# Kernel tuning notes

Measured on AMD Instinct MI355X. Metric: run time of the kernel, lower is better.

Reference implementation:

```python
import jax, jax.numpy as jnp
import numpy as np

TEMPERATURE = 0.5
EPS = 1e-8  # torch CosineSimilarity eps


def setup_inputs() -> dict:
    key = jax.random.key(0)
    k1, k2 = jax.random.split(key)
    N, D = 4096, 256
    z1 = jax.random.normal(k1, (N, D), dtype=jnp.float32)
    z2 = jax.random.normal(k2, (N, D), dtype=jnp.float32)
    return {"z1": z1, "z2": z2}


def reference(z1, z2):
    N = z1.shape[0]
    z = jnp.concatenate([z1, z2], axis=0)  # [2N, D]
    # cosine similarity = normalized dot products (GEMM instead of O(N^2 D) broadcast)
    norm = jnp.linalg.norm(z, axis=-1, keepdims=True)
    zn = z / jnp.maximum(norm, EPS)
    sim = (zn @ zn.T) / TEMPERATURE  # [2N, 2N]
    # mask self-similarity on the diagonal
    idx = jnp.arange(2 * N)
    sim = jnp.where(idx[:, None] == idx[None, :], -jnp.inf, sim)
    # target[i] = (i - N) mod 2N  (arange(2N).roll(N))
    target = jnp.roll(idx, N)
    logp = jax.nn.log_softmax(sim, axis=-1)
    loss = -jnp.mean(logp[idx, target])
    return loss
```

## Files before the change

### kernel.cpp

```cpp
#include <hip/hip_runtime.h>

typedef __bf16 bf16x8 __attribute__((ext_vector_type(8)));
typedef float f32x4 __attribute__((ext_vector_type(4)));

#define TWO_LOG2E 2.88539008177792681f

#define GLOADLDS16(g, l) __builtin_amdgcn_global_load_lds(                     \
    (const __attribute__((address_space(1))) void*)(g),                        \
    (__attribute__((address_space(3))) void*)(l), 16, 0, 0)

__device__ __forceinline__ unsigned f2bf(float f) {
    unsigned u = __float_as_uint(f);
    return (u + 0x7FFFu + ((u >> 16) & 1u)) >> 16;
}

__global__ void __launch_bounds__(256) normalize_kernel(
    const float* __restrict__ z1, const float* __restrict__ z2,
    unsigned short* __restrict__ zn, float* __restrict__ S, float* __restrict__ out)
{
    if (blockIdx.x < 32) S[(blockIdx.x << 8) + threadIdx.x] = 0.f;
    if (blockIdx.x == 32 && threadIdx.x == 0) out[0] = 0.f;

    const int wave = threadIdx.x >> 6, lane = threadIdx.x & 63;
    const int row = (blockIdx.x << 2) + wave;
    const float* src = (row < 4096) ? (z1 + row * 256) : (z2 + (row - 4096) * 256);
    float4 v = ((const float4*)src)[lane];
    float ss = v.x * v.x + v.y * v.y + v.z * v.z + v.w * v.w;
#pragma unroll
    for (int m = 32; m > 0; m >>= 1) ss += __shfl_xor(ss, m, 64);
    float sc = 1.0f / fmaxf(sqrtf(ss), 1e-8f);
    uint2 w;
    w.x = f2bf(v.x * sc) | (f2bf(v.y * sc) << 16);
    w.y = f2bf(v.z * sc) | (f2bf(v.w * sc) << 16);
    *(uint2*)(zn + row * 256 + (lane << 2)) = w;
}

__global__ void __launch_bounds__(64, 2) simexp_kernel(
    const unsigned short* __restrict__ zn, float* __restrict__ S)
{
    __shared__ __align__(16) unsigned short Bs[2][2048];

    const int lane = threadIdx.x;
    const int q = lane >> 4, n16 = lane & 15;
    const int job = blockIdx.x;
    const int rowBase = (job >> 4) << 6;
    const int colRun  = (job & 15) << 9;

    bf16x8 a[4][8];
#pragma unroll
    for (int rt = 0; rt < 4; ++rt)
#pragma unroll
        for (int ks = 0; ks < 8; ++ks)
            a[rt][ks] = *(const bf16x8*)(zn + ((rowBase + (rt << 4) + n16) << 8)
                                            + (ks << 5) + (q << 3));

    auto stage = [&](int m, int buf) {
        const int cc = m >> 2, kc = m & 3;
        const int colBase = colRun + (cc << 5);
        unsigned short* base = &Bs[buf][0];
#pragma unroll
        for (int p = 0; p < 4; ++p) {
            int s = (p << 6) + lane;
            int c = s >> 3, d = s & 7;
            int k8 = d ^ (c & 7);
            GLOADLDS16(zn + ((colBase + c) << 8) + (kc << 6) + (k8 << 3),
                       base + (s << 3));
        }
    };

    float rs[4][4];
#pragma unroll
    for (int i = 0; i < 4; ++i)
#pragma unroll
        for (int j = 0; j < 4; ++j) rs[i][j] = 0.f;

    stage(0, 0);
    int buf = 0;

    for (int cc = 0; cc < 16; ++cc) {
        f32x4 acc[4][2];
#pragma unroll
        for (int rt = 0; rt < 4; ++rt)
#pragma unroll
            for (int ct = 0; ct < 2; ++ct) acc[rt][ct] = (f32x4){0.f, 0.f, 0.f, 0.f};

#pragma unroll
        for (int kc = 0; kc < 4; ++kc) {
            int m = (cc << 2) + kc + 1;
            if (m < 64) {
                stage(m, buf ^ 1);
                asm volatile("s_waitcnt vmcnt(4)" ::: "memory");
            } else {
                asm volatile("s_waitcnt vmcnt(0)" ::: "memory");
            }

            const unsigned short* bb = &Bs[buf][0];
#pragma unroll
            for (int ks = 0; ks < 2; ++ks) {
                bf16x8 bf[2];
#pragma unroll
                for (int ct = 0; ct < 2; ++ct) {
                    int c  = (ct << 4) + n16;
                    int k8 = ((ks << 2) + q) ^ (c & 7);
                    bf[ct] = *(const bf16x8*)(bb + (((c << 3) + k8) << 3));
                }
#pragma unroll
                for (int rt = 0; rt < 4; ++rt)
#pragma unroll
                    for (int ct = 0; ct < 2; ++ct)
                        acc[rt][ct] = __builtin_amdgcn_mfma_f32_16x16x32_bf16(
                            a[rt][(kc << 1) + ks], bf[ct], acc[rt][ct], 0, 0, 0);
            }
            buf ^= 1;
        }

#pragma unroll
        for (int rt = 0; rt < 4; ++rt)
#pragma unroll
            for (int ct = 0; ct < 2; ++ct)
#pragma unroll
                for (int r = 0; r < 4; ++r)
                    rs[rt][r] += __builtin_amdgcn_exp2f(acc[rt][ct][r] * TWO_LOG2E);
    }

#pragma unroll
    for (int rt = 0; rt < 4; ++rt)
#pragma unroll
        for (int r = 0; r < 4; ++r) {
            float s = rs[rt][r];
            s += __shfl_xor(s, 1, 64);
            s += __shfl_xor(s, 2, 64);
            s += __shfl_xor(s, 4, 64);
            s += __shfl_xor(s, 8, 64);
            if (n16 == 0) atomicAdd(&S[rowBase + (rt << 4) + (q << 2) + r], s);
        }
}

__global__ void __launch_bounds__(256) finish_kernel(
    const unsigned short* __restrict__ zn, const float* __restrict__ S,
    float* __restrict__ out)
{
    __shared__ float vals[16];
    const int tid = threadIdx.x, lane = tid & 63, wave = tid >> 6;
    const int q = lane >> 4, n16 = lane & 15;
    const int rib = (wave << 2) + q;
    const int row = (blockIdx.x << 4) + rib;
    const int tar = (row + 4096) & 8191;

    float drr = 0.f, drt = 0.f;
#pragma unroll
    for (int i = 0; i < 4; ++i) {
        int k = (i << 6) + (n16 << 2);
        uint2 ur = *(const uint2*)(zn + (row << 8) + k);
        uint2 ut = *(const uint2*)(zn + (tar << 8) + k);
        float a0 = __uint_as_float(ur.x << 16),  a1 = __uint_as_float(ur.x & 0xFFFF0000u);
        float a2 = __uint_as_float(ur.y << 16),  a3 = __uint_as_float(ur.y & 0xFFFF0000u);
        float b0 = __uint_as_float(ut.x << 16),  b1 = __uint_as_float(ut.x & 0xFFFF0000u);
        float b2 = __uint_as_float(ut.y << 16),  b3 = __uint_as_float(ut.y & 0xFFFF0000u);
        drr += a0 * a0 + a1 * a1 + a2 * a2 + a3 * a3;
        drt += a0 * b0 + a1 * b1 + a2 * b2 + a3 * b3;
    }
#pragma unroll
    for (int m = 1; m <= 8; m <<= 1) {
        drr += __shfl_xor(drr, m, 64);
        drt += __shfl_xor(drt, m, 64);
    }
    if (n16 == 0) {
        float Sv = S[row] - __builtin_amdgcn_exp2f(drr * TWO_LOG2E);
        vals[rib] = 0.693147180559945f * __builtin_amdgcn_logf(Sv) - 2.0f * drt;
    }
    __syncthreads();
    if (tid == 0) {
        float s = 0.f;
#pragma unroll
        for (int i = 0; i < 16; ++i) s += vals[i];
        atomicAdd(out, s * (1.0f / 8192.0f));
    }
}

extern "C" void kernel_launch(void* const* d_in, const int* in_sizes, int n_in,
                              void* d_out, int out_size, void* d_ws, size_t ws_size,
                              hipStream_t stream)
{
    const float* z1 = (const float*)d_in[0];
    const float* z2 = (const float*)d_in[1];
    unsigned short* zn = (unsigned short*)d_ws;
    float* S = (float*)((char*)d_ws + 8192 * 256 * sizeof(unsigned short));
    float* out = (float*)d_out;

    normalize_kernel<<<2048, 256, 0, stream>>>(z1, z2, zn, S, out);
    simexp_kernel<<<2048, 64, 0, stream>>>(zn, S);
    finish_kernel<<<512, 256, 0, stream>>>(zn, S, out);
}
```

Baseline: 107.1 us.

## Fuse three kernels into one cooperative kernel with grid syncs and triple-buffered LDS

Merges the normalize, similarity-exp and finish kernels into a single cooperative launch of 2048 single-wave blocks, separated by grid-wide syncs, with a fallback to three separate launches. The goal is to remove the launch gaps between kernels. It also changes the B-tile staging from double to triple buffering with a deeper vmcnt wait, to hide more global-to-LDS latency. In exchange it pays for two grid barriers and host-side attribute and occupancy queries on every call. It also needs all 2048 blocks to be resident at once, and the occupancy check decides whether the fused path or the fallback runs.

```diff
diff --git a/kernel.cpp b/kernel.cpp
--- a/kernel.cpp
+++ b/kernel.cpp
@@ -1,4 +1,7 @@
 #include <hip/hip_runtime.h>
+#include <hip/hip_cooperative_groups.h>
+
+namespace cg = cooperative_groups;
 
 typedef __bf16 bf16x8 __attribute__((ext_vector_type(8)));
 typedef float f32x4 __attribute__((ext_vector_type(4)));
@@ -14,32 +17,34 @@
     return (u + 0x7FFFu + ((u >> 16) & 1u)) >> 16;
 }
 
-__global__ void __launch_bounds__(256) normalize_kernel(
-    const float* __restrict__ z1, const float* __restrict__ z2,
-    unsigned short* __restrict__ zn, float* __restrict__ S, float* __restrict__ out)
-{
-    if (blockIdx.x < 32) S[(blockIdx.x << 8) + threadIdx.x] = 0.f;
-    if (blockIdx.x == 32 && threadIdx.x == 0) out[0] = 0.f;
-
-    const int wave = threadIdx.x >> 6, lane = threadIdx.x & 63;
-    const int row = (blockIdx.x << 2) + wave;
-    const float* src = (row < 4096) ? (z1 + row * 256) : (z2 + (row - 4096) * 256);
-    float4 v = ((const float4*)src)[lane];
-    float ss = v.x * v.x + v.y * v.y + v.z * v.z + v.w * v.w;
-#pragma unroll
-    for (int m = 32; m > 0; m >>= 1) ss += __shfl_xor(ss, m, 64);
-    float sc = 1.0f / fmaxf(sqrtf(ss), 1e-8f);
-    uint2 w;
-    w.x = f2bf(v.x * sc) | (f2bf(v.y * sc) << 16);
-    w.y = f2bf(v.z * sc) | (f2bf(v.w * sc) << 16);
-    *(uint2*)(zn + row * 256 + (lane << 2)) = w;
-}
-
-__global__ void __launch_bounds__(64, 2) simexp_kernel(
-    const unsigned short* __restrict__ zn, float* __restrict__ S)
-{
-    __shared__ __align__(16) unsigned short Bs[2][2048];
-
+__device__ __forceinline__ void phase1(const float* __restrict__ z1,
+                                       const float* __restrict__ z2,
+                                       unsigned short* __restrict__ zn,
+                                       float* __restrict__ S,
+                                       float* __restrict__ out) {
+    const int lane = threadIdx.x;
+    const int b = blockIdx.x;
+    if (lane < 4) S[(b << 2) + lane] = 0.f;
+    if (b == 0 && lane == 0) out[0] = 0.f;
+#pragma unroll
+    for (int r = 0; r < 4; ++r) {
+        int row = (b << 2) + r;
+        const float* src = (row < 4096) ? (z1 + row * 256) : (z2 + (row - 4096) * 256);
+        float4 v = ((const float4*)src)[lane];
+        float ss = v.x * v.x + v.y * v.y + v.z * v.z + v.w * v.w;
+#pragma unroll
+        for (int m = 32; m > 0; m >>= 1) ss += __shfl_xor(ss, m, 64);
+        float sc = 1.0f / fmaxf(sqrtf(ss), 1e-8f);
+        uint2 w;
+        w.x = f2bf(v.x * sc) | (f2bf(v.y * sc) << 16);
+        w.y = f2bf(v.z * sc) | (f2bf(v.w * sc) << 16);
+        *(uint2*)(zn + row * 256 + (lane << 2)) = w;
+    }
+}
+
+__device__ __forceinline__ void phase2(const unsigned short* __restrict__ zn,
+                                       float* __restrict__ S,
+                                       unsigned short* __restrict__ Bs) {
     const int lane = threadIdx.x;
     const int q = lane >> 4, n16 = lane & 15;
     const int job = blockIdx.x;
@@ -54,17 +59,16 @@
             a[rt][ks] = *(const bf16x8*)(zn + ((rowBase + (rt << 4) + n16) << 8)
                                             + (ks << 5) + (q << 3));
 
-    auto stage = [&](int m, int buf) {
-        const int cc = m >> 2, kc = m & 3;
-        const int colBase = colRun + (cc << 5);
-        unsigned short* base = &Bs[buf][0];
+    auto stage = [&](int m, int off) {
+        const int colBase = colRun + ((m >> 2) << 5);
+        const int koff = (m & 3) << 6;
+        unsigned short* base = Bs + off;
 #pragma unroll
         for (int p = 0; p < 4; ++p) {
             int s = (p << 6) + lane;
             int c = s >> 3, d = s & 7;
             int k8 = d ^ (c & 7);
-            GLOADLDS16(zn + ((colBase + c) << 8) + (kc << 6) + (k8 << 3),
-                       base + (s << 3));
+            GLOADLDS16(zn + ((colBase + c) << 8) + koff + (k8 << 3), base + (s << 3));
         }
     };
 
@@ -74,46 +78,27 @@
 #pragma unroll
         for (int j = 0; j < 4; ++j) rs[i][j] = 0.f;
 
-    stage(0, 0);
-    int buf = 0;
-
-    for (int cc = 0; cc < 16; ++cc) {
-        f32x4 acc[4][2];
-#pragma unroll
-        for (int rt = 0; rt < 4; ++rt)
-#pragma unroll
-            for (int ct = 0; ct < 2; ++ct) acc[rt][ct] = (f32x4){0.f, 0.f, 0.f, 0.f};
-
-#pragma unroll
-        for (int kc = 0; kc < 4; ++kc) {
-            int m = (cc << 2) + kc + 1;
-            if (m < 64) {
-                stage(m, buf ^ 1);
-                asm volatile("s_waitcnt vmcnt(4)" ::: "memory");
-            } else {
-                asm volatile("s_waitcnt vmcnt(0)" ::: "memory");
+    f32x4 acc[4][2];
+    auto consume = [&](int off, int kc) {
+        const unsigned short* bb = Bs + off;
+#pragma unroll
+        for (int ks = 0; ks < 2; ++ks) {
+            bf16x8 bf[2];
+#pragma unroll
+            for (int ct = 0; ct < 2; ++ct) {
+                int c  = (ct << 4) + n16;
+                int k8 = ((ks << 2) + q) ^ (c & 7);
+                bf[ct] = *(const bf16x8*)(bb + (((c << 3) + k8) << 3));
             }
-
-            const unsigned short* bb = &Bs[buf][0];
-#pragma unroll
-            for (int ks = 0; ks < 2; ++ks) {
-                bf16x8 bf[2];
-#pragma unroll
-                for (int ct = 0; ct < 2; ++ct) {
-                    int c  = (ct << 4) + n16;
-                    int k8 = ((ks << 2) + q) ^ (c & 7);
-                    bf[ct] = *(const bf16x8*)(bb + (((c << 3) + k8) << 3));
-                }
-#pragma unroll
-                for (int rt = 0; rt < 4; ++rt)
-#pragma unroll
-                    for (int ct = 0; ct < 2; ++ct)
-                        acc[rt][ct] = __builtin_amdgcn_mfma_f32_16x16x32_bf16(
-                            a[rt][(kc << 1) + ks], bf[ct], acc[rt][ct], 0, 0, 0);
-            }
-            buf ^= 1;
-        }
-
+#pragma unroll
+            for (int rt = 0; rt < 4; ++rt)
+#pragma unroll
+                for (int ct = 0; ct < 2; ++ct)
+                    acc[rt][ct] = __builtin_amdgcn_mfma_f32_16x16x32_bf16(
+                        a[rt][(kc << 1) + ks], bf[ct], acc[rt][ct], 0, 0, 0);
+        }
+    };
+    auto epilogue = [&]() {
 #pragma unroll
         for (int rt = 0; rt < 4; ++rt)
 #pragma unroll
@@ -121,7 +106,48 @@
 #pragma unroll
                 for (int r = 0; r < 4; ++r)
                     rs[rt][r] += __builtin_amdgcn_exp2f(acc[rt][ct][r] * TWO_LOG2E);
-    }
+    };
+
+    stage(0, 0);
+    stage(1, 2048);
+    int mp = 2;
+    int off_p = 4096, off_c = 0;
+
+    for (int cc = 0; cc < 15; ++cc) {
+#pragma unroll
+        for (int rt = 0; rt < 4; ++rt)
+#pragma unroll
+            for (int ct = 0; ct < 2; ++ct) acc[rt][ct] = (f32x4){0.f, 0.f, 0.f, 0.f};
+#pragma unroll
+        for (int kc = 0; kc < 4; ++kc) {
+            stage(mp, off_p);
+            asm volatile("s_waitcnt vmcnt(8)" ::: "memory");
+            consume(off_c, kc);
+            ++mp;
+            off_p += 2048; if (off_p == 6144) off_p = 0;
+            off_c += 2048; if (off_c == 6144) off_c = 0;
+        }
+        epilogue();
+    }
+#pragma unroll
+    for (int rt = 0; rt < 4; ++rt)
+#pragma unroll
+        for (int ct = 0; ct < 2; ++ct) acc[rt][ct] = (f32x4){0.f, 0.f, 0.f, 0.f};
+    stage(62, off_p);
+    asm volatile("s_waitcnt vmcnt(8)" ::: "memory");
+    consume(off_c, 0);
+    off_p += 2048; if (off_p == 6144) off_p = 0;
+    off_c += 2048; if (off_c == 6144) off_c = 0;
+    stage(63, off_p);
+    asm volatile("s_waitcnt vmcnt(8)" ::: "memory");
+    consume(off_c, 1);
+    off_c += 2048; if (off_c == 6144) off_c = 0;
+    asm volatile("s_waitcnt vmcnt(4)" ::: "memory");
+    consume(off_c, 2);
+    off_c += 2048; if (off_c == 6144) off_c = 0;
+    asm volatile("s_waitcnt vmcnt(0)" ::: "memory");
+    consume(off_c, 3);
+    epilogue();
 
 #pragma unroll
     for (int rt = 0; rt < 4; ++rt)
@@ -136,21 +162,19 @@
         }
 }
 
-__global__ void __launch_bounds__(256) finish_kernel(
-    const unsigned short* __restrict__ zn, const float* __restrict__ S,
-    float* __restrict__ out)
-{
-    __shared__ float vals[16];
-    const int tid = threadIdx.x, lane = tid & 63, wave = tid >> 6;
+__device__ __forceinline__ void phase3(const unsigned short* __restrict__ zn,
+                                       const float* __restrict__ S,
+                                       float* __restrict__ out) {
+    const int lane = threadIdx.x;
     const int q = lane >> 4, n16 = lane & 15;
-    const int rib = (wave << 2) + q;
-    const int row = (blockIdx.x << 4) + rib;
+    const int b = blockIdx.x;
+    const int row = (b << 2) + q;
     const int tar = (row + 4096) & 8191;
 
     float drr = 0.f, drt = 0.f;
 #pragma unroll
     for (int i = 0; i < 4; ++i) {
-        int k = (i << 6) + (n16 << 2);
+        int k = (n16 << 4) + (i << 2);
         uint2 ur = *(const uint2*)(zn + (row << 8) + k);
         uint2 ut = *(const uint2*)(zn + (tar << 8) + k);
         float a0 = __uint_as_float(ur.x << 16),  a1 = __uint_as_float(ur.x & 0xFFFF0000u);
@@ -165,18 +189,44 @@
         drr += __shfl_xor(drr, m, 64);
         drt += __shfl_xor(drt, m, 64);
     }
+    float val = 0.f;
     if (n16 == 0) {
         float Sv = S[row] - __builtin_amdgcn_exp2f(drr * TWO_LOG2E);
-        vals[rib] = 0.693147180559945f * __builtin_amdgcn_logf(Sv) - 2.0f * drt;
-    }
-    __syncthreads();
-    if (tid == 0) {
-        float s = 0.f;
-#pragma unroll
-        for (int i = 0; i < 16; ++i) s += vals[i];
-        atomicAdd(out, s * (1.0f / 8192.0f));
-    }
-}
+        val = 0.693147180559945f * __builtin_amdgcn_logf(Sv) - 2.0f * drt;
+    }
+    val += __shfl_xor(val, 16, 64);
+    val += __shfl_xor(val, 32, 64);
+    if (lane == 0) atomicAdd(out, val * (1.0f / 8192.0f));
+}
+
+__global__ void __launch_bounds__(64, 2) ntxent_fused(
+    const float* __restrict__ z1, const float* __restrict__ z2,
+    unsigned short* __restrict__ zn, float* __restrict__ S, float* __restrict__ out)
+{
+    __shared__ __align__(16) unsigned short Bs[3][2048];
+    phase1(z1, z2, zn, S, out);
+    cg::this_grid().sync();
+    phase2(zn, S, &Bs[0][0]);
+    cg::this_grid().sync();
+    phase3(zn, S, out);
+}
+
+__global__ void __launch_bounds__(64) norm_k(
+    const float* __restrict__ z1, const float* __restrict__ z2,
+    unsigned short* __restrict__ zn, float* __restrict__ S, float* __restrict__ out)
+{ phase1(z1, z2, zn, S, out); }
+
+__global__ void __launch_bounds__(64, 2) simexp_k(
+    const unsigned short* __restrict__ zn, float* __restrict__ S)
+{
+    __shared__ __align__(16) unsigned short Bs[3][2048];
+    phase2(zn, S, &Bs[0][0]);
+}
+
+__global__ void __launch_bounds__(64) finish_k(
+    const unsigned short* __restrict__ zn, const float* __restrict__ S,
+    float* __restrict__ out)
+{ phase3(zn, S, out); }
 
 extern "C" void kernel_launch(void* const* d_in, const int* in_sizes, int n_in,
                               void* d_out, int out_size, void* d_ws, size_t ws_size,
@@ -188,7 +238,22 @@
     float* S = (float*)((char*)d_ws + 8192 * 256 * sizeof(unsigned short));
     float* out = (float*)d_out;
 
-    normalize_kernel<<<2048, 256, 0, stream>>>(z1, z2, zn, S, out);
-    simexp_kernel<<<2048, 64, 0, stream>>>(zn, S);
-    finish_kernel<<<512, 256, 0, stream>>>(zn, S, out);
-}
+    int dev = 0;
+    hipGetDevice(&dev);
+    int coopOK = 0;
+    hipDeviceGetAttribute(&coopOK, hipDeviceAttributeCooperativeLaunch, dev);
+    int cus = 0;
+    hipDeviceGetAttribute(&cus, hipDeviceAttributeMultiprocessorCount, dev);
+    int maxB = 0;
+    hipOccupancyMaxActiveBlocksPerMultiprocessor(&maxB, ntxent_fused, 64, 0);
+
+    if (coopOK && (long long)maxB * cus >= 2048) {
+        void* args[] = {(void*)&z1, (void*)&z2, (void*)&zn, (void*)&S, (void*)&out};
+        hipError_t err = hipLaunchCooperativeKernel(ntxent_fused, dim3(2048), dim3(64),
+                                                    args, 0, stream);
+        if (err == hipSuccess) return;
+    }
+    norm_k<<<2048, 64, 0, stream>>>(z1, z2, zn, S, out);
+    simexp_k<<<2048, 64, 0, stream>>>(zn, S);
+    finish_k<<<2048, 64, 0, stream>>>(zn, S, out);
+}
```

New measurement: 127.1 us. 18.7% more time.

## Deepen simexp LDS pipeline to four smaller buffers with three-stage prefetch

Applied to the files above, without the earlier changes.

Splits the B-tile staging into 32-wide K chunks held in a four-slot LDS ring, keeping three global-to-LDS loads in flight ahead of consumption instead of one. The swizzle is changed to a 4-way XOR to match the narrower rows. The aim is to hide global load latency better for the single-wave blocks at the same LDS footprint. In exchange it adds more wait points and smaller per-stage transfers, and relies on ordering to avoid overwriting a slot still being read.

```diff
diff --git a/kernel.cpp b/kernel.cpp
--- a/kernel.cpp
+++ b/kernel.cpp
@@ -38,7 +38,7 @@
 __global__ void __launch_bounds__(64, 2) simexp_kernel(
     const unsigned short* __restrict__ zn, float* __restrict__ S)
 {
-    __shared__ __align__(16) unsigned short Bs[2][2048];
+    __shared__ __align__(16) unsigned short Bs[4][1024];
 
     const int lane = threadIdx.x;
     const int q = lane >> 4, n16 = lane & 15;
@@ -54,17 +54,16 @@
             a[rt][ks] = *(const bf16x8*)(zn + ((rowBase + (rt << 4) + n16) << 8)
                                             + (ks << 5) + (q << 3));
 
-    auto stage = [&](int m, int buf) {
-        const int cc = m >> 2, kc = m & 3;
-        const int colBase = colRun + (cc << 5);
-        unsigned short* base = &Bs[buf][0];
-#pragma unroll
-        for (int p = 0; p < 4; ++p) {
+    auto stage = [&](int m) {
+        const int colBase = colRun + ((m >> 3) << 5);
+        const int koff = (m & 7) << 5;
+        unsigned short* base = (unsigned short*)&Bs[0][0] + ((m & 3) << 10);
+#pragma unroll
+        for (int p = 0; p < 2; ++p) {
             int s = (p << 6) + lane;
-            int c = s >> 3, d = s & 7;
-            int k8 = d ^ (c & 7);
-            GLOADLDS16(zn + ((colBase + c) << 8) + (kc << 6) + (k8 << 3),
-                       base + (s << 3));
+            int c = s >> 2, d = s & 3;
+            int k8 = d ^ (c & 3);
+            GLOADLDS16(zn + ((colBase + c) << 8) + koff + (k8 << 3), base + (s << 3));
         }
     };
 
@@ -74,46 +73,31 @@
 #pragma unroll
         for (int j = 0; j < 4; ++j) rs[i][j] = 0.f;
 
-    stage(0, 0);
-    int buf = 0;
-
-    for (int cc = 0; cc < 16; ++cc) {
-        f32x4 acc[4][2];
+    f32x4 acc[4][2];
+    auto consume = [&](int m) {
+        const unsigned short* bb = (const unsigned short*)&Bs[0][0] + ((m & 3) << 10);
+        const int kc = m & 7;
+        bf16x8 bf[2];
+#pragma unroll
+        for (int ct = 0; ct < 2; ++ct) {
+            int c = (ct << 4) + n16;
+            int d = q ^ (c & 3);
+            bf[ct] = *(const bf16x8*)(bb + (((c << 2) | d) << 3));
+        }
 #pragma unroll
         for (int rt = 0; rt < 4; ++rt)
 #pragma unroll
+            for (int ct = 0; ct < 2; ++ct)
+                acc[rt][ct] = __builtin_amdgcn_mfma_f32_16x16x32_bf16(
+                    a[rt][kc], bf[ct], acc[rt][ct], 0, 0, 0);
+    };
+    auto acczero = [&]() {
+#pragma unroll
+        for (int rt = 0; rt < 4; ++rt)
+#pragma unroll
             for (int ct = 0; ct < 2; ++ct) acc[rt][ct] = (f32x4){0.f, 0.f, 0.f, 0.f};
-
-#pragma unroll
-        for (int kc = 0; kc < 4; ++kc) {
-            int m = (cc << 2) + kc + 1;
-            if (m < 64) {
-                stage(m, buf ^ 1);
-                asm volatile("s_waitcnt vmcnt(4)" ::: "memory");
-            } else {
-                asm volatile("s_waitcnt vmcnt(0)" ::: "memory");
-            }
-
-            const unsigned short* bb = &Bs[buf][0];
-#pragma unroll
-            for (int ks = 0; ks < 2; ++ks) {
-                bf16x8 bf[2];
-#pragma unroll
-                for (int ct = 0; ct < 2; ++ct) {
-                    int c  = (ct << 4) + n16;
-                    int k8 = ((ks << 2) + q) ^ (c & 7);
-                    bf[ct] = *(const bf16x8*)(bb + (((c << 3) + k8) << 3));
-                }
-#pragma unroll
-                for (int rt = 0; rt < 4; ++rt)
-#pragma unroll
-                    for (int ct = 0; ct < 2; ++ct)
-                        acc[rt][ct] = __builtin_amdgcn_mfma_f32_16x16x32_bf16(
-                            a[rt][(kc << 1) + ks], bf[ct], acc[rt][ct], 0, 0, 0);
-            }
-            buf ^= 1;
-        }
-
+    };
+    auto epilogue = [&]() {
 #pragma unroll
         for (int rt = 0; rt < 4; ++rt)
 #pragma unroll
@@ -121,7 +105,36 @@
 #pragma unroll
                 for (int r = 0; r < 4; ++r)
                     rs[rt][r] += __builtin_amdgcn_exp2f(acc[rt][ct][r] * TWO_LOG2E);
-    }
+    };
+
+    stage(0); stage(1); stage(2);
+
+    for (int cc = 0; cc < 15; ++cc) {
+        acczero();
+#pragma unroll
+        for (int kc = 0; kc < 8; ++kc) {
+            int m = (cc << 3) + kc;
+            stage(m + 3);
+            asm volatile("s_waitcnt vmcnt(6)" ::: "memory");
+            consume(m);
+        }
+        epilogue();
+    }
+    acczero();
+#pragma unroll
+    for (int kc = 0; kc < 5; ++kc) {
+        int m = 120 + kc;
+        stage(m + 3);
+        asm volatile("s_waitcnt vmcnt(6)" ::: "memory");
+        consume(m);
+    }
+    asm volatile("s_waitcnt vmcnt(4)" ::: "memory");
+    consume(125);
+    asm volatile("s_waitcnt vmcnt(2)" ::: "memory");
+    consume(126);
+    asm volatile("s_waitcnt vmcnt(0)" ::: "memory");
+    consume(127);
+    epilogue();
 
 #pragma unroll
     for (int rt = 0; rt < 4; ++rt)
```

Measured after the change: 106.8 us. Within noise of the previous version (-0.3%).

## Pre-pack normalized rows into MFMA fragment layout and drop LDS staging

Applied to the files above, without the earlier changes.

The normalize kernel now also writes a second copy of the bf16 normalized matrix, rearranged into 16-row blocks whose layout matches the MFMA operand fragments. The sim-exp kernel then loads B fragments straight from global memory (through the cache) with contiguous 16-byte loads, removing the LDS double buffer, global_load_lds staging and waitcnt pipelining. This removes the LDS traffic and swizzle arithmetic, but it relies on L2/cache hits and loop unrolling to hide global latency instead of explicit prefetch. It also adds an extra 4 MB workspace write.

```diff
diff --git a/kernel.cpp b/kernel.cpp
--- a/kernel.cpp
+++ b/kernel.cpp
@@ -5,18 +5,16 @@
 
 #define TWO_LOG2E 2.88539008177792681f
 
-#define GLOADLDS16(g, l) __builtin_amdgcn_global_load_lds(                     \
-    (const __attribute__((address_space(1))) void*)(g),                        \
-    (__attribute__((address_space(3))) void*)(l), 16, 0, 0)
-
 __device__ __forceinline__ unsigned f2bf(float f) {
     unsigned u = __float_as_uint(f);
     return (u + 0x7FFFu + ((u >> 16) & 1u)) >> 16;
 }
 
+
 __global__ void __launch_bounds__(256) normalize_kernel(
     const float* __restrict__ z1, const float* __restrict__ z2,
-    unsigned short* __restrict__ zn, float* __restrict__ S, float* __restrict__ out)
+    unsigned short* __restrict__ zn, unsigned short* __restrict__ znB,
+    float* __restrict__ S, float* __restrict__ out)
 {
     if (blockIdx.x < 32) S[(blockIdx.x << 8) + threadIdx.x] = 0.f;
     if (blockIdx.x == 32 && threadIdx.x == 0) out[0] = 0.f;
@@ -33,40 +31,27 @@
     w.x = f2bf(v.x * sc) | (f2bf(v.y * sc) << 16);
     w.y = f2bf(v.z * sc) | (f2bf(v.w * sc) << 16);
     *(uint2*)(zn + row * 256 + (lane << 2)) = w;
+    *(uint2*)(znB + ((row >> 4) << 12) + ((lane >> 3) << 9) + ((row & 15) << 5)
+                  + (((lane >> 1) & 3) << 3) + ((lane & 1) << 2)) = w;
 }
 
 __global__ void __launch_bounds__(64, 2) simexp_kernel(
-    const unsigned short* __restrict__ zn, float* __restrict__ S)
+    const unsigned short* __restrict__ znB, float* __restrict__ S)
 {
-    __shared__ __align__(16) unsigned short Bs[2][2048];
-
     const int lane = threadIdx.x;
     const int q = lane >> 4, n16 = lane & 15;
+    const int lp = (((n16 << 2) | q) << 3);
     const int job = blockIdx.x;
     const int rowBase = (job >> 4) << 6;
-    const int colRun  = (job & 15) << 9;
+    const int run = job & 15;
 
     bf16x8 a[4][8];
 #pragma unroll
     for (int rt = 0; rt < 4; ++rt)
 #pragma unroll
         for (int ks = 0; ks < 8; ++ks)
-            a[rt][ks] = *(const bf16x8*)(zn + ((rowBase + (rt << 4) + n16) << 8)
-                                            + (ks << 5) + (q << 3));
-
-    auto stage = [&](int m, int buf) {
-        const int cc = m >> 2, kc = m & 3;
-        const int colBase = colRun + (cc << 5);
-        unsigned short* base = &Bs[buf][0];
-#pragma unroll
-        for (int p = 0; p < 4; ++p) {
-            int s = (p << 6) + lane;
-            int c = s >> 3, d = s & 7;
-            int k8 = d ^ (c & 7);
-            GLOADLDS16(zn + ((colBase + c) << 8) + (kc << 6) + (k8 << 3),
-                       base + (s << 3));
-        }
-    };
+            a[rt][ks] = *(const bf16x8*)(znB + ((((rowBase >> 4) + rt)) << 12)
+                                             + (ks << 9) + lp);
 
     float rs[4][4];
 #pragma unroll
@@ -74,53 +59,31 @@
 #pragma unroll
         for (int j = 0; j < 4; ++j) rs[i][j] = 0.f;
 
-    stage(0, 0);
-    int buf = 0;
+    const unsigned short* bbase = znB + ((run << 5) << 12);
 
-    for (int cc = 0; cc < 16; ++cc) {
-        f32x4 acc[4][2];
+#pragma unroll 2
+    for (int cg = 0; cg < 32; ++cg) {
+        const unsigned short* gb = bbase + (cg << 12);
+        bf16x8 b[8];
 #pragma unroll
-        for (int rt = 0; rt < 4; ++rt)
+        for (int ks = 0; ks < 8; ++ks)
+            b[ks] = *(const bf16x8*)(gb + (ks << 9) + lp);
+
+        f32x4 acc[4];
 #pragma unroll
-            for (int ct = 0; ct < 2; ++ct) acc[rt][ct] = (f32x4){0.f, 0.f, 0.f, 0.f};
-
+        for (int rt = 0; rt < 4; ++rt) acc[rt] = (f32x4){0.f, 0.f, 0.f, 0.f};
 #pragma unroll
-        for (int kc = 0; kc < 4; ++kc) {
-            int m = (cc << 2) + kc + 1;
-            if (m < 64) {
-                stage(m, buf ^ 1);
-                asm volatile("s_waitcnt vmcnt(4)" ::: "memory");
-            } else {
-                asm volatile("s_waitcnt vmcnt(0)" ::: "memory");
-            }
-
-            const unsigned short* bb = &Bs[buf][0];
+        for (int ks = 0; ks < 8; ++ks)
 #pragma unroll
-            for (int ks = 0; ks < 2; ++ks) {
-                bf16x8 bf[2];
-#pragma unroll
-                for (int ct = 0; ct < 2; ++ct) {
-                    int c  = (ct << 4) + n16;
-                    int k8 = ((ks << 2) + q) ^ (c & 7);
-                    bf[ct] = *(const bf16x8*)(bb + (((c << 3) + k8) << 3));
-                }
-#pragma unroll
-                for (int rt = 0; rt < 4; ++rt)
-#pragma unroll
-                    for (int ct = 0; ct < 2; ++ct)
-                        acc[rt][ct] = __builtin_amdgcn_mfma_f32_16x16x32_bf16(
-                            a[rt][(kc << 1) + ks], bf[ct], acc[rt][ct], 0, 0, 0);
-            }
-            buf ^= 1;
-        }
+            for (int rt = 0; rt < 4; ++rt)
+                acc[rt] = __builtin_amdgcn_mfma_f32_16x16x32_bf16(
+                    a[rt][ks], b[ks], acc[rt], 0, 0, 0);
 
 #pragma unroll
         for (int rt = 0; rt < 4; ++rt)
 #pragma unroll
-            for (int ct = 0; ct < 2; ++ct)
-#pragma unroll
-                for (int r = 0; r < 4; ++r)
-                    rs[rt][r] += __builtin_amdgcn_exp2f(acc[rt][ct][r] * TWO_LOG2E);
+            for (int r = 0; r < 4; ++r)
+                rs[rt][r] += __builtin_amdgcn_exp2f(acc[rt][r] * TWO_LOG2E);
     }
 
 #pragma unroll
@@ -184,11 +147,12 @@
 {
     const float* z1 = (const float*)d_in[0];
     const float* z2 = (const float*)d_in[1];
-    unsigned short* zn = (unsigned short*)d_ws;
-    float* S = (float*)((char*)d_ws + 8192 * 256 * sizeof(unsigned short));
+    unsigned short* zn  = (unsigned short*)d_ws;
+    unsigned short* znB = zn + 8192 * 256;
+    float* S = (float*)((char*)d_ws + 2 * 8192 * 256 * sizeof(unsigned short));
     float* out = (float*)d_out;
 
-    normalize_kernel<<<2048, 256, 0, stream>>>(z1, z2, zn, S, out);
-    simexp_kernel<<<2048, 64, 0, stream>>>(zn, S);
+    normalize_kernel<<<2048, 256, 0, stream>>>(z1, z2, zn, znB, S, out);
+    simexp_kernel<<<2048, 64, 0, stream>>>(znB, S);
     finish_kernel<<<512, 256, 0, stream>>>(zn, S, out);
 }
```

Result: slower. 112.3 us (+4.9%).
